# Optimization experiments

Measured on AMD Instinct MI355X. Metric: run time of the kernel, lower is better.

## Reference

```python
import jax, jax.numpy as jnp
import numpy as np

N, E, G = 10000, 80000, 32
Z, C, B, H = 10, 128, 8, 64
R_MAX = 5.0
AVG_NEIGH = 16.0
L_OFF = [0, 1, 4, 9, 16]  # slice offsets for l = 0..3 blocks of the SH vector


def real_sh(u):
    # Real spherical harmonics up to l=3, 'component' normalization (sum_m Y_lm^2 = 2l+1)
    x, y, z = u[:, 0], u[:, 1], u[:, 2]
    s3, s5, s15 = 3.0 ** 0.5, 5.0 ** 0.5, 15.0 ** 0.5
    cols = [
        jnp.ones_like(x),
        s3 * x, s3 * y, s3 * z,
        s15 * x * y, s15 * y * z, (s5 / 2) * (3 * z ** 2 - 1),
        s15 * x * z, (s15 / 2) * (x ** 2 - y ** 2),
        (70.0 ** 0.5 / 4) * (3 * x ** 2 * y - y ** 3),
        105.0 ** 0.5 * x * y * z,
        (42.0 ** 0.5 / 4) * y * (5 * z ** 2 - 1),
        (7.0 ** 0.5 / 2) * (5 * z ** 3 - 3 * z),
        (42.0 ** 0.5 / 4) * x * (5 * z ** 2 - 1),
        (105.0 ** 0.5 / 2) * z * (x ** 2 - y ** 2),
        (70.0 ** 0.5 / 4) * (x ** 3 - 3 * x * y ** 2),
    ]
    return jnp.stack(cols, axis=-1)  # [E, 16]


def poly_cutoff(x, p=5):
    f = (1.0 - (p + 1) * (p + 2) / 2 * x ** p
         + p * (p + 2) * x ** (p + 1)
         - p * (p + 1) / 2 * x ** (p + 2))
    return f * (x < 1.0).astype(f.dtype)


def setup_inputs() -> dict:
    key = jax.random.key(0)
    ks = jax.random.split(key, 20)
    vectors = jax.random.normal(ks[0], (E, 3), dtype=jnp.float32) * 1.5
    elem = jax.random.randint(ks[1], (N,), 0, Z)
    node_attrs = jax.nn.one_hot(elem, Z, dtype=jnp.float32)
    edge_index = jax.random.randint(ks[2], (2, E), 0, N).astype(jnp.int64)
    batch = jnp.sort(jax.random.randint(ks[3], (N,), 0, G)).astype(jnp.int64)

    def init(k, shape, fan_in):
        return jax.random.normal(k, shape, dtype=jnp.float32) / np.sqrt(fan_in)

    return {
        "vectors": vectors,
        "node_attrs": node_attrs,
        "W_embed": init(ks[4], (Z, C), Z),
        "atomic_energies": -jnp.arange(1, Z + 1, dtype=jnp.float32),
        "rw1": init(ks[5], (2, B, H), B),
        "rw2": init(ks[6], (2, H, H), H),
        "rw3": init(ks[7], (2, H, H), H),
        "rw4": init(ks[8], (2, H, 4 * C), H),
        "Wmix": init(ks[9], (2, 4, C, C), C),
        "U": init(ks[10], (2, Z, 4), Z),
        "Wprod": init(ks[11], (2, C, C), C),
        "Wsc": init(ks[12], (2, C, C), C),
        "Wro0": init(ks[13], (C, 1), C),
        "Wro1a": init(ks[14], (C, 16), C),
        "Wro1b": init(ks[15], (16, 1), 16),
        "scale": jnp.array([1.0], dtype=jnp.float32),
        "shift": jnp.array([0.0], dtype=jnp.float32),
        "edge_index": edge_index,
        "batch": batch,
    }


def reference(vectors, node_attrs, W_embed, atomic_energies, rw1, rw2, rw3, rw4,
              Wmix, U, Wprod, Wsc, Wro0, Wro1a, Wro1b, scale, shift,
              edge_index, batch):
    sender, receiver = edge_index[0], edge_index[1]
    r = jnp.linalg.norm(vectors, axis=-1)                     # [E]
    u = vectors / r[:, None]
    Y = real_sh(u)                                            # [E, 16]
    n = jnp.arange(1, B + 1, dtype=vectors.dtype)
    bessel = jnp.sqrt(2.0 / R_MAX) * jnp.sin(n[None] * jnp.pi * r[:, None] / R_MAX) / r[:, None]
    edge_feats = bessel * poly_cutoff(r / R_MAX)[:, None]     # [E, B]

    h = node_attrs @ W_embed                                  # [N, C] node embedding
    node_e0 = node_attrs @ atomic_energies                    # [N] atomic reference energies
    e0 = jax.ops.segment_sum(node_e0, batch, num_segments=G)  # [G]

    node_inter = jnp.zeros((node_attrs.shape[0],), dtype=vectors.dtype)
    for i in range(2):  # interaction layers (fixed small count)
        f = jax.nn.silu(edge_feats @ rw1[i])
        f = jax.nn.silu(f @ rw2[i])
        f = jax.nn.silu(f @ rw3[i])
        R_w = (f @ rw4[i]).reshape(-1, 4, C)                  # [E, 4, C] radial weights per l-path
        hs = h[sender]                                        # [E, C] edge gather
        A_parts = []
        for l in range(4):
            # channelwise tensor product (uvu): scalar node feats x Y_l -> l
            m = (R_w[:, l, :] * hs)[:, :, None] * Y[:, None, L_OFF[l]:L_OFF[l + 1]]  # [E, C, 2l+1]
            agg = jax.ops.segment_sum(m, receiver, num_segments=node_attrs.shape[0]) / AVG_NEIGH
            A_parts.append(jnp.einsum('ncm,cd->ndm', agg, Wmix[i, l]))
        # product basis: rotation-invariant powers per l, element-dependent contraction
        inv = jnp.stack([(p ** 2).sum(-1) for p in A_parts], axis=-1)  # [N, C, 4]
        w = node_attrs @ U[i]                                          # [N, 4]
        h = jnp.einsum('ncl,nl->nc', inv, w) @ Wprod[i] + h @ Wsc[i]   # product + residual sc
        if i == 0:
            node_inter = node_inter + (h @ Wro0)[:, 0]                 # linear readout
        else:
            node_inter = node_inter + (jax.nn.silu(h @ Wro1a) @ Wro1b)[:, 0]  # nonlinear readout
    node_inter = scale[0] * node_inter + shift[0]                       # scale-shift
    total = e0 + jax.ops.segment_sum(node_inter, batch, num_segments=G)
    return total  # [G] per-graph energies
```

## Files before the change

kernel.cpp:

```cpp
#include <hip/hip_runtime.h>

#define NN 10000
#define NE 80000
#define NG 32
#define NZ 10
#define NC 128
#define RMAXF 5.0f

typedef _Float16 f16;
typedef _Float16 half8 __attribute__((ext_vector_type(8)));
typedef float f32x4 __attribute__((ext_vector_type(4)));

__device__ __forceinline__ float silu_f(float x) {
    return x / (1.0f + __expf(-x));
}

__device__ __forceinline__ int clampi(int v, int lo, int hi) {
    return v < lo ? lo : (v > hi ? hi : v);
}

__device__ __forceinline__ uint4 pack8f(float4 a, float4 b) {
    union { f16 h[8]; uint4 u; } P;
    P.h[0] = (f16)a.x; P.h[1] = (f16)a.y; P.h[2] = (f16)a.z; P.h[3] = (f16)a.w;
    P.h[4] = (f16)b.x; P.h[5] = (f16)b.y; P.h[6] = (f16)b.z; P.h[7] = (f16)b.w;
    return P.u;
}

__global__ void zero_stuff(int* counts, int* cursor, float* out) {
    int i = blockIdx.x * blockDim.x + threadIdx.x;
    if (i < NN) { counts[i] = 0; cursor[i] = 0; }
    if (i < NG) out[i] = 0.0f;
}

__global__ void prep_weights(const float* __restrict__ Wmix, const float* __restrict__ Wprod,
                             const float* __restrict__ Wsc,
                             const float* __restrict__ rw2, const float* __restrict__ rw3,
                             const float* __restrict__ rw4,
                             f16* __restrict__ WmixT, f16* __restrict__ WprodT, f16* __restrict__ WscT,
                             f16* __restrict__ w2T, f16* __restrict__ w3T, f16* __restrict__ w4T) {
    int i = blockIdx.x * blockDim.x + threadIdx.x;
    if (i < 2 * 4 * 128 * 128) {
        int cc = i & 127, d = (i >> 7) & 127, g = i >> 14;
        WmixT[i] = (f16)Wmix[((size_t)g * 128 + cc) * 128 + d];
    }
    if (i < 2 * 128 * 128) {
        int cc = i & 127, d = (i >> 7) & 127, g = i >> 14;
        WprodT[i] = (f16)Wprod[((size_t)g * 128 + cc) * 128 + d];
        WscT[i]   = (f16)Wsc[((size_t)g * 128 + cc) * 128 + d];
    }
    if (i < 2 * 512 * 64) {
        int k = i & 63, j = (i >> 6) & 511, ly = i >> 15;
        w4T[i] = (f16)rw4[((size_t)ly * 64 + k) * 512 + j];
    }
    if (i < 2 * 64 * 64) {
        int k = i & 63, j = (i >> 6) & 63, ly = i >> 12;
        w2T[i] = (f16)rw2[((size_t)ly * 64 + k) * 64 + j];
        w3T[i] = (f16)rw3[((size_t)ly * 64 + k) * 64 + j];
    }
}

__global__ void node_init(const float* __restrict__ attrs, const float* __restrict__ W_embed,
                          const float* __restrict__ ae, const float* __restrict__ U,
                          float* __restrict__ h, float* __restrict__ node_e0, float* __restrict__ wU) {
    int gid = blockIdx.x * blockDim.x + threadIdx.x;
    if (gid >= NN * NC) return;
    int n = gid >> 7, c = gid & 127;
    float a[NZ];
#pragma unroll
    for (int z = 0; z < NZ; z++) a[z] = attrs[n * NZ + z];
    float acc = 0.f;
#pragma unroll
    for (int z = 0; z < NZ; z++) acc += a[z] * W_embed[z * NC + c];
    h[(size_t)n * NC + c] = acc;
    if (c == 0) {
        float e = 0.f;
#pragma unroll
        for (int z = 0; z < NZ; z++) e += a[z] * ae[z];
        node_e0[n] = e;
    }
    if (c < 8) {
        int i = c >> 2, l = c & 3;
        float s = 0.f;
#pragma unroll
        for (int z = 0; z < NZ; z++) s += a[z] * U[i * NZ * 4 + z * 4 + l];
        wU[(size_t)i * NN * 4 + n * 4 + l] = s;
    }
}

__global__ void edge_geom(const float* __restrict__ vec, float* __restrict__ Y, float* __restrict__ ef) {
    int e = blockIdx.x * blockDim.x + threadIdx.x;
    if (e >= NE) return;
    float vx = vec[e * 3 + 0], vy = vec[e * 3 + 1], vz = vec[e * 3 + 2];
    float r = sqrtf(vx * vx + vy * vy + vz * vz);
    float inv = 1.0f / r;
    float x = vx * inv, y = vy * inv, z = vz * inv;
    const float s3 = 1.7320508075688772f;
    const float s5 = 2.23606797749979f;
    const float s15 = 3.872983346207417f;
    const float c9 = 2.091650066335189f;
    const float c10 = 10.246950765959598f;
    const float c11 = 1.6201851746019651f;
    const float c12 = 1.3228756555322954f;
    const float c14 = 5.123475382979799f;
    float o[16];
    o[0] = 1.0f;
    o[1] = s3 * x; o[2] = s3 * y; o[3] = s3 * z;
    o[4] = s15 * x * y; o[5] = s15 * y * z; o[6] = 0.5f * s5 * (3.f * z * z - 1.f);
    o[7] = s15 * x * z; o[8] = 0.5f * s15 * (x * x - y * y);
    o[9] = c9 * (3.f * x * x * y - y * y * y);
    o[10] = c10 * x * y * z;
    o[11] = c11 * y * (5.f * z * z - 1.f);
    o[12] = c12 * (5.f * z * z * z - 3.f * z);
    o[13] = c11 * x * (5.f * z * z - 1.f);
    o[14] = c14 * z * (x * x - y * y);
    o[15] = c9 * (x * x * x - 3.f * x * y * y);
#pragma unroll
    for (int m = 0; m < 16; m++) Y[(size_t)e * 16 + m] = o[m];
    float xc = r / RMAXF;
    float cut = 0.0f;
    if (xc < 1.0f) {
        float x5 = xc * xc * xc * xc * xc;
        cut = 1.0f - 21.0f * x5 + 35.0f * x5 * xc - 15.0f * x5 * xc * xc;
    }
    float pref = sqrtf(2.0f / RMAXF) * inv * cut;
#pragma unroll
    for (int b = 0; b < 8; b++) {
        float arg = (float)(b + 1) * 3.14159265358979323846f * r / RMAXF;
        ef[(size_t)e * 8 + b] = pref * sinf(arg);
    }
}

__global__ void hist_recv(const int* __restrict__ recv, int* __restrict__ counts) {
    int e = blockIdx.x * blockDim.x + threadIdx.x;
    if (e < NE) atomicAdd(&counts[clampi(recv[e], 0, NN - 1)], 1);
}

__global__ void scan_counts(const int* __restrict__ counts, int* __restrict__ rowstart) {
    __shared__ int part[1024];
    int t = threadIdx.x;
    const int CH = 10;
    int base = t * CH;
    int loc[CH];
    int s = 0;
#pragma unroll
    for (int j = 0; j < CH; j++) {
        int v = (base + j < NN) ? counts[base + j] : 0;
        loc[j] = s; s += v;
    }
    part[t] = s;
    __syncthreads();
    for (int off = 1; off < 1024; off <<= 1) {
        int v = (t >= off) ? part[t - off] : 0;
        __syncthreads();
        part[t] += v;
        __syncthreads();
    }
    int chunk = (t > 0) ? part[t - 1] : 0;
#pragma unroll
    for (int j = 0; j < CH; j++)
        if (base + j < NN) rowstart[base + j] = chunk + loc[j];
    if (t == 0) rowstart[NN] = part[1023];
}

__global__ void scatter_edges(const int* __restrict__ recv, const int* __restrict__ rowstart,
                              int* __restrict__ cursor, int* __restrict__ elist) {
    int e = blockIdx.x * blockDim.x + threadIdx.x;
    if (e < NE) {
        int r = clampi(recv[e], 0, NN - 1);
        int p = atomicAdd(&cursor[r], 1);
        int slot = clampi(rowstart[r] + p, 0, NE - 1);
        elist[slot] = e;
    }
}

__global__ __launch_bounds__(256) void edge_mlp(const float* __restrict__ ef,
                                                const float* __restrict__ w1,
                                                const f16* __restrict__ w2T, const f16* __restrict__ w3T,
                                                const f16* __restrict__ w4T,
                                                f16* __restrict__ Rw) {
    __shared__ __align__(16) char L[8192 * 2 + 16384];
    char* X1 = L;
    char* X2 = L + 8192;
    char* X4 = L + 16384;

    int tid = threadIdx.x;
    int lane = tid & 63;
    int w = tid >> 6;
    int ln = lane & 15, kq = lane >> 4;
    int eb = blockIdx.x * 64;

    {
        int jb = w * 16;
        const float4* efv = (const float4*)(ef + (size_t)(eb + lane) * 8);
        float4 ea = efv[0], eb4 = efv[1];
        float in8[8] = {ea.x, ea.y, ea.z, ea.w, eb4.x, eb4.y, eb4.z, eb4.w};
        f16 pk[16];
#pragma unroll
        for (int j = 0; j < 16; j++) {
            float a = 0.f;
#pragma unroll
            for (int b = 0; b < 8; b++) a += in8[b] * w1[b * 64 + jb + j];
            pk[j] = (f16)silu_f(a);
        }
        int base = lane * 128 + jb * 2;
#pragma unroll
        for (int t = 0; t < 2; t++) {
            int byte = (base + t * 16) ^ ((lane & 7) << 4);
            *(uint4*)(X1 + byte) = ((uint4*)pk)[t];
        }
    }
    __syncthreads();

    {
        half8 a[2];
#pragma unroll
        for (int kc = 0; kc < 2; kc++) {
            int byte = ((w * 16 + ln) * 128 + kc * 64 + kq * 16) ^ ((ln & 7) << 4);
            a[kc] = *(const half8*)(X1 + byte);
        }
#pragma unroll
        for (int nt = 0; nt < 4; nt++) {
            f32x4 acc = {0.f, 0.f, 0.f, 0.f};
#pragma unroll
            for (int kc = 0; kc < 2; kc++) {
                half8 b = *(const half8*)(w2T + (nt * 16 + ln) * 64 + kc * 32 + kq * 8);
                acc = __builtin_amdgcn_mfma_f32_16x16x32_f16(a[kc], b, acc, 0, 0, 0);
            }
#pragma unroll
            for (int r = 0; r < 4; r++) {
                int row = w * 16 + kq * 4 + r;
                int byte = (row * 128 + (nt * 16 + ln) * 2) ^ ((row & 7) << 4);
                *(f16*)(X2 + byte) = (f16)silu_f(acc[r]);
            }
        }
    }
    __syncthreads();

    {
        half8 a[2];
#pragma unroll
        for (int kc = 0; kc < 2; kc++) {
            int byte = ((w * 16 + ln) * 128 + kc * 64 + kq * 16) ^ ((ln & 7) << 4);
            a[kc] = *(const half8*)(X2 + byte);
        }
#pragma unroll
        for (int nt = 0; nt < 4; nt++) {
            f32x4 acc = {0.f, 0.f, 0.f, 0.f};
#pragma unroll
            for (int kc = 0; kc < 2; kc++) {
                half8 b = *(const half8*)(w3T + (nt * 16 + ln) * 64 + kc * 32 + kq * 8);
                acc = __builtin_amdgcn_mfma_f32_16x16x32_f16(a[kc], b, acc, 0, 0, 0);
            }
#pragma unroll
            for (int r = 0; r < 4; r++) {
                int row = w * 16 + kq * 4 + r;
                int byte = (row * 128 + (nt * 16 + ln) * 2) ^ ((row & 7) << 4);
                *(f16*)(X1 + byte) = (f16)silu_f(acc[r]);
            }
        }
    }
    __syncthreads();

    half8 a3[2];
#pragma unroll
    for (int kc = 0; kc < 2; kc++) {
        int byte = ((w * 16 + ln) * 128 + kc * 64 + kq * 16) ^ ((ln & 7) << 4);
        a3[kc] = *(const half8*)(X1 + byte);
    }
    for (int q = 0; q < 4; q++) {
#pragma unroll
        for (int nt = 0; nt < 8; nt++) {
            f32x4 acc = {0.f, 0.f, 0.f, 0.f};
#pragma unroll
            for (int kc = 0; kc < 2; kc++) {
                half8 b = *(const half8*)(w4T + ((q * 8 + nt) * 16 + ln) * 64 + kc * 32 + kq * 8);
                acc = __builtin_amdgcn_mfma_f32_16x16x32_f16(a3[kc], b, acc, 0, 0, 0);
            }
#pragma unroll
            for (int r = 0; r < 4; r++) {
                int row = w * 16 + kq * 4 + r;
                int byte = (row * 256 + (nt * 16 + ln) * 2) ^ ((row & 15) << 4);
                *(f16*)(X4 + byte) = (f16)acc[r];
            }
        }
#pragma unroll
        for (int it = 0; it < 4; it++) {
            int i = it * 64 + lane;
            int row = w * 16 + (i >> 4);
            int chunk = i & 15;
            int byte = (row * 256 + chunk * 16) ^ ((row & 15) << 4);
            uint4 v = *(const uint4*)(X4 + byte);
            *(uint4*)(Rw + (size_t)(eb + row) * 512 + q * 128 + chunk * 8) = v;
        }
    }
}

__global__ __launch_bounds__(256) void agg_only(const int* __restrict__ rowstart, const int* __restrict__ elist,
                                                const int* __restrict__ send, const float* __restrict__ h_in,
                                                const f16* __restrict__ Rw, const float* __restrict__ Y,
                                                f16* __restrict__ aggH) {
    __shared__ int eL[64], sL[64];
    int n = blockIdx.x, tid = threadIdx.x;
    int c = tid & 127, mh = tid >> 7;
    float acc[8];
#pragma unroll
    for (int q = 0; q < 8; q++) acc[q] = 0.f;
    int beg = rowstart[n], end = rowstart[n + 1];
    for (int base = beg; base < end; base += 64) {
        int cnt = min(64, end - base);
        __syncthreads();
        if (tid < cnt) {
            int e = clampi(elist[base + tid], 0, NE - 1);
            eL[tid] = e;
            sL[tid] = clampi(send[e], 0, NN - 1);
        }
        __syncthreads();
        for (int idx = 0; idx < cnt; idx++) {
            int e = eL[idx];
            int s = sL[idx];
            float hs = h_in[(size_t)s * NC + c];
            const f16* rwp = Rw + (size_t)e * 512;
            float y[8];
#pragma unroll
            for (int q = 0; q < 8; q++) y[q] = Y[(size_t)e * 16 + mh * 8 + q];
            if (mh == 0) {
                float p0 = (float)rwp[c] * hs;
                float p1 = (float)rwp[128 + c] * hs;
                float p2 = (float)rwp[256 + c] * hs;
                acc[0] += p0 * y[0];
                acc[1] += p1 * y[1]; acc[2] += p1 * y[2]; acc[3] += p1 * y[3];
                acc[4] += p2 * y[4]; acc[5] += p2 * y[5]; acc[6] += p2 * y[6]; acc[7] += p2 * y[7];
            } else {
                float p2 = (float)rwp[256 + c] * hs;
                float p3 = (float)rwp[384 + c] * hs;
                acc[0] += p2 * y[0];
#pragma unroll
                for (int q = 1; q < 8; q++) acc[q] += p3 * y[q];
            }
        }
    }
    const float inv16 = 1.0f / 16.0f;
#pragma unroll
    for (int q = 0; q < 8; q++)
        aggH[(size_t)n * 2048 + (size_t)(mh * 8 + q) * NC + c] = (f16)(acc[q] * inv16);
}

__global__ __launch_bounds__(512) void mix_mfma(
    const f16* __restrict__ aggH, const f16* __restrict__ WmixT,
    const float* __restrict__ wU, const float* __restrict__ h_in,
    const f16* __restrict__ WprodT, const f16* __restrict__ WscT,
    const float* __restrict__ Wro0, const float* __restrict__ Wro1a, const float* __restrict__ Wro1b,
    float* __restrict__ h_out, float* __restrict__ ni, int layer)
{
    __shared__ __align__(16) char Lb[32768];
    float* invwL = (float*)(Lb);
    f16*   invwH = (f16*)(Lb + 8192);
    f16*   hH    = (f16*)(Lb + 12288);
    f16*   houtH = (f16*)(Lb + 16384);
    float* p16L  = (float*)(Lb + 20480);

    int tid = threadIdx.x;
    int nb = blockIdx.x * 16;
    int lane = tid & 63;
    int w = tid >> 6;
    int ln = lane & 15, kq = lane >> 4;

    float4 wUreg[4];
#pragma unroll
    for (int r = 0; r < 4; r++)
        wUreg[r] = *(const float4*)(wU + (size_t)(nb + kq * 4 + r) * 4);

    float invwacc[4] = {0.f, 0.f, 0.f, 0.f};

#pragma unroll
    for (int g = 0; g < 4; g++) {
        const int mstart = (g == 0) ? 0 : (g == 1) ? 1 : (g == 2) ? 4 : 9;
        const int mend   = (g == 0) ? 1 : (g == 1) ? 4 : (g == 2) ? 9 : 16;
        {
            const uint4* src = (const uint4*)(WmixT + ((size_t)(layer * 4 + g) << 14));
#pragma unroll
            for (int it = 0; it < 4; it++) {
                int i = it * 512 + tid;
                int row = i >> 4, col = i & 15;
                int byte = (row * 256 + col * 16) ^ ((row & 7) << 4);
                *(uint4*)(Lb + byte) = src[i];
            }
        }
        __syncthreads();
#pragma unroll
        for (int m = mstart; m < mend; m++) {
            half8 a[4];
            const f16* arow = aggH + (size_t)(nb + ln) * 2048 + m * 128 + kq * 8;
#pragma unroll
            for (int k = 0; k < 4; k++) a[k] = *(const half8*)(arow + k * 32);
            f32x4 acc = {0.f, 0.f, 0.f, 0.f};
#pragma unroll
            for (int k = 0; k < 4; k++) {
                int row = w * 16 + ln;
                int byte = (row * 256 + k * 64 + kq * 16) ^ ((row & 7) << 4);
                half8 b = *(const half8*)(Lb + byte);
                acc = __builtin_amdgcn_mfma_f32_16x16x32_f16(a[k], b, acc, 0, 0, 0);
            }
            float wu = (g == 0) ? wUreg[0].x : (g == 1) ? wUreg[0].y : (g == 2) ? wUreg[0].z : wUreg[0].w;
#pragma unroll
            for (int r = 0; r < 4; r++) {
                float wur = (g == 0) ? wUreg[r].x : (g == 1) ? wUreg[r].y : (g == 2) ? wUreg[r].z : wUreg[r].w;
                invwacc[r] += acc[r] * acc[r] * wur;
            }
            (void)wu;
        }
        __syncthreads();
    }

#pragma unroll
    for (int r = 0; r < 4; r++)
        invwL[(kq * 4 + r) * 128 + w * 16 + ln] = invwacc[r];
    __syncthreads();

    if (tid < 256) {
        int node = tid >> 4, ch = tid & 15;
        int byte = (node * 256 + ch * 16) ^ ((node & 7) << 4);
        float4 v0 = *(float4*)&invwL[node * 128 + ch * 8];
        float4 v1 = *(float4*)&invwL[node * 128 + ch * 8 + 4];
        *(uint4*)((char*)invwH + byte) = pack8f(v0, v1);
        const float4* hp = (const float4*)(h_in + (size_t)(nb + node) * 128 + ch * 8);
        float4 g0 = hp[0], g1 = hp[1];
        *(uint4*)((char*)hH + byte) = pack8f(g0, g1);
    }
    __syncthreads();

    {
        half8 ai[4], ah[4];
#pragma unroll
        for (int k = 0; k < 4; k++) {
            int byte = (ln * 256 + (k * 32 + kq * 8) * 2) ^ ((ln & 7) << 4);
            ai[k] = *(const half8*)((char*)invwH + byte);
            ah[k] = *(const half8*)((char*)hH + byte);
        }
        const f16* Bp = WprodT + ((size_t)layer << 14);
        const f16* Bs = WscT + ((size_t)layer << 14);
        f32x4 acc = {0.f, 0.f, 0.f, 0.f};
#pragma unroll
        for (int k = 0; k < 4; k++) {
            half8 b = *(const half8*)(Bp + (w * 16 + ln) * 128 + k * 32 + kq * 8);
            acc = __builtin_amdgcn_mfma_f32_16x16x32_f16(ai[k], b, acc, 0, 0, 0);
        }
#pragma unroll
        for (int k = 0; k < 4; k++) {
            half8 b = *(const half8*)(Bs + (w * 16 + ln) * 128 + k * 32 + kq * 8);
            acc = __builtin_amdgcn_mfma_f32_16x16x32_f16(ah[k], b, acc, 0, 0, 0);
        }
#pragma unroll
        for (int r = 0; r < 4; r++) {
            int node = kq * 4 + r;
            int d = w * 16 + ln;
            h_out[(size_t)(nb + node) * 128 + d] = acc[r];
            houtH[node * 128 + d] = (f16)acc[r];
        }
    }
    __syncthreads();

    if (tid < 256) {
        int rn = tid >> 4, rj = tid & 15;
        if (layer == 0) {
            float s = 0.f;
            for (int cc = rj; cc < 128; cc += 16) s += (float)houtH[rn * 128 + cc] * Wro0[cc];
            p16L[tid] = s;
        } else {
            float s = 0.f;
            for (int cc = 0; cc < 128; cc++) s += (float)houtH[rn * 128 + cc] * Wro1a[cc * 16 + rj];
            s = silu_f(s);
            p16L[tid] = s * Wro1b[rj];
        }
    }
    __syncthreads();
    if (tid < 16) {
        float t = 0.f;
#pragma unroll
        for (int j = 0; j < 16; j++) t += p16L[tid * 16 + j];
        ni[nb + tid] = (layer == 0) ? t : (ni[nb + tid] + t);
    }
}

__global__ void finalize(const float* __restrict__ node_e0, const float* __restrict__ ni,
                         const int* __restrict__ batch, const float* __restrict__ scale,
                         const float* __restrict__ shift, float* __restrict__ out) {
    __shared__ float bins[NG];
    int tid = threadIdx.x;
    if (tid < NG) bins[tid] = 0.f;
    __syncthreads();
    int n = blockIdx.x * blockDim.x + tid;
    if (n < NN) {
        float v = node_e0[n] + scale[0] * ni[n] + shift[0];
        atomicAdd(&bins[clampi(batch[n], 0, NG - 1)], v);
    }
    __syncthreads();
    if (tid < NG) atomicAdd(&out[tid], bins[tid]);
}

extern "C" void kernel_launch(void* const* d_in, const int* in_sizes, int n_in,
                              void* d_out, int out_size, void* d_ws, size_t ws_size,
                              hipStream_t stream) {
    (void)in_sizes; (void)n_in; (void)out_size; (void)ws_size;
    const float* vectors = (const float*)d_in[0];
    const float* attrs   = (const float*)d_in[1];
    const float* W_embed = (const float*)d_in[2];
    const float* ae      = (const float*)d_in[3];
    const float* rw1     = (const float*)d_in[4];
    const float* rw2     = (const float*)d_in[5];
    const float* rw3     = (const float*)d_in[6];
    const float* rw4     = (const float*)d_in[7];
    const float* Wmix    = (const float*)d_in[8];
    const float* U       = (const float*)d_in[9];
    const float* Wprod   = (const float*)d_in[10];
    const float* Wsc     = (const float*)d_in[11];
    const float* Wro0    = (const float*)d_in[12];
    const float* Wro1a   = (const float*)d_in[13];
    const float* Wro1b   = (const float*)d_in[14];
    const float* scale   = (const float*)d_in[15];
    const float* shift   = (const float*)d_in[16];
    const int* eidx      = (const int*)d_in[17];
    const int* batch     = (const int*)d_in[18];
    float* out = (float*)d_out;

    char* w = (char*)d_ws;
    size_t off = 0;
    auto alloc = [&](size_t bytes) -> void* {
        void* p = (void*)(w + off);
        off += (bytes + 255) & ~(size_t)255;
        return p;
    };
    float* Y       = (float*)alloc((size_t)NE * 16 * 4);
    float* ef      = (float*)alloc((size_t)NE * 8 * 4);
    f16*   Rw      = (f16*)  alloc((size_t)NE * 512 * 2);
    f16*   aggH    = (f16*)  alloc((size_t)NN * 2048 * 2);
    float* hA      = (float*)alloc((size_t)NN * NC * 4);
    float* hB      = (float*)alloc((size_t)NN * NC * 4);
    float* wU      = (float*)alloc((size_t)2 * NN * 4 * 4);
    float* node_e0 = (float*)alloc((size_t)NN * 4);
    float* ni      = (float*)alloc((size_t)NN * 4);
    f16*   WmixT   = (f16*)  alloc((size_t)2 * 4 * 128 * 128 * 2);
    f16*   WprodT  = (f16*)  alloc((size_t)2 * 128 * 128 * 2);
    f16*   WscT    = (f16*)  alloc((size_t)2 * 128 * 128 * 2);
    f16*   w2T     = (f16*)  alloc((size_t)2 * 64 * 64 * 2);
    f16*   w3T     = (f16*)  alloc((size_t)2 * 64 * 64 * 2);
    f16*   w4T     = (f16*)  alloc((size_t)2 * 512 * 64 * 2);
    int* counts    = (int*)alloc((size_t)NN * 4);
    int* rowstart  = (int*)alloc((size_t)(NN + 1) * 4);
    int* cursor    = (int*)alloc((size_t)NN * 4);
    int* elist     = (int*)alloc((size_t)NE * 4);

    const int* send = eidx;
    const int* recv = eidx + NE;
    zero_stuff<<<(NN + 255) / 256, 256, 0, stream>>>(counts, cursor, out);
    prep_weights<<<512, 256, 0, stream>>>(Wmix, Wprod, Wsc, rw2, rw3, rw4,
                                          WmixT, WprodT, WscT, w2T, w3T, w4T);
    node_init<<<(NN * NC + 255) / 256, 256, 0, stream>>>(attrs, W_embed, ae, U, hA, node_e0, wU);
    edge_geom<<<(NE + 255) / 256, 256, 0, stream>>>(vectors, Y, ef);
    hist_recv<<<(NE + 255) / 256, 256, 0, stream>>>(recv, counts);
    scan_counts<<<1, 1024, 0, stream>>>(counts, rowstart);
    scatter_edges<<<(NE + 255) / 256, 256, 0, stream>>>(recv, rowstart, cursor, elist);

    float* hcur = hA;
    float* hnext = hB;
    for (int layer = 0; layer < 2; layer++) {
        edge_mlp<<<NE / 64, 256, 0, stream>>>(
            ef, rw1 + layer * 8 * 64,
            w2T + (size_t)layer * 64 * 64, w3T + (size_t)layer * 64 * 64,
            w4T + (size_t)layer * 512 * 64, Rw);
        agg_only<<<NN, 256, 0, stream>>>(rowstart, elist, send, hcur, Rw, Y, aggH);
        mix_mfma<<<NN / 16, 512, 0, stream>>>(
            aggH, WmixT, wU + (size_t)layer * NN * 4, hcur,
            WprodT, WscT, Wro0, Wro1a, Wro1b, hnext, ni, layer);
        float* t = hcur; hcur = hnext; hnext = t;
    }
    finalize<<<(NN + 255) / 256, 256, 0, stream>>>(node_e0, ni, batch, scale, shift, out);
}
```

Before: 354.8 us.

## Fuse edge radial MLP with receiver-sorted aggregation to drop Rw buffer

Replaces the separate edge_mlp and agg_only kernels with one edge_agg kernel. Each block takes the edges of a contiguous range of receiver nodes in sorted order, computes their radial MLP weights in shared memory, and accumulates the messages per node directly into aggH. This removes the global write and re-read of the large per-edge Rw tensor, which is 512 f16 values per edge, in every layer. A new nstart_build kernel maps blocks to node ranges. It also adds an f16 copy of h to halve sender-feature gather traffic. In exchange, the MLP is computed over a padded 128-edge tile per block even when fewer edges are present. The aggregation walks edges one at a time inside each block, and edge loads now go through an indirection.

New measurement: 447.4 us. 1.26x slower.

```diff
diff --git a/kernel.cpp b/kernel.cpp
--- a/kernel.cpp
+++ b/kernel.cpp
@@ -5,10 +5,12 @@
 #define NG 32
 #define NZ 10
 #define NC 128
+#define NB (NE / 64)
 #define RMAXF 5.0f
 
 typedef _Float16 f16;
 typedef _Float16 half8 __attribute__((ext_vector_type(8)));
+typedef _Float16 half4 __attribute__((ext_vector_type(4)));
 typedef float f32x4 __attribute__((ext_vector_type(4)));
 
 __device__ __forceinline__ float silu_f(float x) {
@@ -61,7 +63,8 @@
 
 __global__ void node_init(const float* __restrict__ attrs, const float* __restrict__ W_embed,
                           const float* __restrict__ ae, const float* __restrict__ U,
-                          float* __restrict__ h, float* __restrict__ node_e0, float* __restrict__ wU) {
+                          float* __restrict__ h, f16* __restrict__ h16,
+                          float* __restrict__ node_e0, float* __restrict__ wU) {
     int gid = blockIdx.x * blockDim.x + threadIdx.x;
     if (gid >= NN * NC) return;
     int n = gid >> 7, c = gid & 127;
@@ -72,6 +75,7 @@
 #pragma unroll
     for (int z = 0; z < NZ; z++) acc += a[z] * W_embed[z * NC + c];
     h[(size_t)n * NC + c] = acc;
+    h16[(size_t)n * NC + c] = (f16)acc;
     if (c == 0) {
         float e = 0.f;
 #pragma unroll
@@ -173,25 +177,61 @@
     }
 }
 
-__global__ __launch_bounds__(256) void edge_mlp(const float* __restrict__ ef,
-                                                const float* __restrict__ w1,
-                                                const f16* __restrict__ w2T, const f16* __restrict__ w3T,
-                                                const f16* __restrict__ w4T,
-                                                f16* __restrict__ Rw) {
-    __shared__ __align__(16) char L[8192 * 2 + 16384];
-    char* X1 = L;
-    char* X2 = L + 8192;
-    char* X4 = L + 16384;
+__global__ void nstart_build(const int* __restrict__ rowstart, int* __restrict__ nstart) {
+    int n = blockIdx.x * blockDim.x + threadIdx.x;
+    if (n > NN) return;
+    int b  = (n == NN) ? NB : clampi(rowstart[n] >> 6, 0, NB - 1);
+    int bp = (n == 0) ? -1 : clampi(rowstart[n - 1] >> 6, 0, NB - 1);
+    for (int bb = bp + 1; bb <= b; bb++) nstart[bb] = n;
+}
+
+__global__ __launch_bounds__(512) void edge_agg(
+    const float* __restrict__ ef, const float* __restrict__ w1,
+    const f16* __restrict__ w2T, const f16* __restrict__ w3T, const f16* __restrict__ w4T,
+    const int* __restrict__ rowstart, const int* __restrict__ nstart,
+    const int* __restrict__ elist, const int* __restrict__ send,
+    const f16* __restrict__ h16, const float* __restrict__ Y,
+    f16* __restrict__ aggH)
+{
+    __shared__ __align__(16) char L[54272];
+    char* X1  = L;
+    char* X2  = L + 16384;
+    char* RwC = L + 32768;
+    f16*  yL  = (f16*)(L + 49152);
+    int*  eL  = (int*)(L + 53248);
+    int*  sL  = (int*)(L + 53760);
+
+    int b = blockIdx.x;
+    int n0 = nstart[b], n1 = nstart[b + 1];
+    if (n0 >= n1) return;
+    int e_beg = rowstart[n0];
+    int cnt = rowstart[n1] - e_beg;
+    if (cnt > 128) cnt = 128;
 
     int tid = threadIdx.x;
     int lane = tid & 63;
     int w = tid >> 6;
     int ln = lane & 15, kq = lane >> 4;
-    int eb = blockIdx.x * 64;
-
+
+    if (tid < 128) {
+        int src = e_beg + ((tid < cnt) ? tid : 0);
+        if (src > NE - 1) src = NE - 1;
+        int e = clampi(elist[src], 0, NE - 1);
+        eL[tid] = e;
+        sL[tid] = clampi(send[e], 0, NN - 1);
+    }
+    __syncthreads();
+
+    for (int idx = tid; idx < 2048; idx += 512) {
+        int i = idx >> 4, m = idx & 15;
+        yL[idx] = (f16)Y[(size_t)eL[i] * 16 + m];
+    }
     {
-        int jb = w * 16;
-        const float4* efv = (const float4*)(ef + (size_t)(eb + lane) * 8);
+        int e_i = tid & 127;
+        int q4 = tid >> 7;
+        int jb = q4 * 16;
+        int ge = eL[e_i];
+        const float4* efv = (const float4*)(ef + (size_t)ge * 8);
         float4 ea = efv[0], eb4 = efv[1];
         float in8[8] = {ea.x, ea.y, ea.z, ea.w, eb4.x, eb4.y, eb4.z, eb4.w};
         f16 pk[16];
@@ -199,13 +239,13 @@
         for (int j = 0; j < 16; j++) {
             float a = 0.f;
 #pragma unroll
-            for (int b = 0; b < 8; b++) a += in8[b] * w1[b * 64 + jb + j];
+            for (int bb = 0; bb < 8; bb++) a += in8[bb] * w1[bb * 64 + jb + j];
             pk[j] = (f16)silu_f(a);
         }
-        int base = lane * 128 + jb * 2;
+        int base = e_i * 128 + jb * 2;
 #pragma unroll
         for (int t = 0; t < 2; t++) {
-            int byte = (base + t * 16) ^ ((lane & 7) << 4);
+            int byte = (base + t * 16) ^ ((e_i & 7) << 4);
             *(uint4*)(X1 + byte) = ((uint4*)pk)[t];
         }
     }
@@ -215,7 +255,8 @@
         half8 a[2];
 #pragma unroll
         for (int kc = 0; kc < 2; kc++) {
-            int byte = ((w * 16 + ln) * 128 + kc * 64 + kq * 16) ^ ((ln & 7) << 4);
+            int row = w * 16 + ln;
+            int byte = (row * 128 + kc * 64 + kq * 16) ^ ((row & 7) << 4);
             a[kc] = *(const half8*)(X1 + byte);
         }
 #pragma unroll
@@ -223,8 +264,8 @@
             f32x4 acc = {0.f, 0.f, 0.f, 0.f};
 #pragma unroll
             for (int kc = 0; kc < 2; kc++) {
-                half8 b = *(const half8*)(w2T + (nt * 16 + ln) * 64 + kc * 32 + kq * 8);
-                acc = __builtin_amdgcn_mfma_f32_16x16x32_f16(a[kc], b, acc, 0, 0, 0);
+                half8 bb = *(const half8*)(w2T + (nt * 16 + ln) * 64 + kc * 32 + kq * 8);
+                acc = __builtin_amdgcn_mfma_f32_16x16x32_f16(a[kc], bb, acc, 0, 0, 0);
             }
 #pragma unroll
             for (int r = 0; r < 4; r++) {
@@ -240,7 +281,8 @@
         half8 a[2];
 #pragma unroll
         for (int kc = 0; kc < 2; kc++) {
-            int byte = ((w * 16 + ln) * 128 + kc * 64 + kq * 16) ^ ((ln & 7) << 4);
+            int row = w * 16 + ln;
+            int byte = (row * 128 + kc * 64 + kq * 16) ^ ((row & 7) << 4);
             a[kc] = *(const half8*)(X2 + byte);
         }
 #pragma unroll
@@ -248,8 +290,8 @@
             f32x4 acc = {0.f, 0.f, 0.f, 0.f};
 #pragma unroll
             for (int kc = 0; kc < 2; kc++) {
-                half8 b = *(const half8*)(w3T + (nt * 16 + ln) * 64 + kc * 32 + kq * 8);
-                acc = __builtin_amdgcn_mfma_f32_16x16x32_f16(a[kc], b, acc, 0, 0, 0);
+                half8 bb = *(const half8*)(w3T + (nt * 16 + ln) * 64 + kc * 32 + kq * 8);
+                acc = __builtin_amdgcn_mfma_f32_16x16x32_f16(a[kc], bb, acc, 0, 0, 0);
             }
 #pragma unroll
             for (int r = 0; r < 4; r++) {
@@ -259,90 +301,87 @@
             }
         }
     }
-    __syncthreads();
-
-    half8 a3[2];
-#pragma unroll
-    for (int kc = 0; kc < 2; kc++) {
-        int byte = ((w * 16 + ln) * 128 + kc * 64 + kq * 16) ^ ((ln & 7) << 4);
-        a3[kc] = *(const half8*)(X1 + byte);
-    }
-    for (int q = 0; q < 4; q++) {
-#pragma unroll
-        for (int nt = 0; nt < 8; nt++) {
-            f32x4 acc = {0.f, 0.f, 0.f, 0.f};
+
+    int c = tid & 127;
+    int mq = tid >> 7;
+    float acc0 = 0.f, acc1 = 0.f, acc2 = 0.f, acc3 = 0.f;
+    int nCur = n0;
+    int rsN = rowstart[nCur + 1];
+    const float inv16 = 0.0625f;
+
+    for (int ec = 0; ec < 8; ec++) {
+        __syncthreads();
+        {
+            half8 a[2];
 #pragma unroll
             for (int kc = 0; kc < 2; kc++) {
-                half8 b = *(const half8*)(w4T + ((q * 8 + nt) * 16 + ln) * 64 + kc * 32 + kq * 8);
-                acc = __builtin_amdgcn_mfma_f32_16x16x32_f16(a3[kc], b, acc, 0, 0, 0);
-            }
-#pragma unroll
-            for (int r = 0; r < 4; r++) {
-                int row = w * 16 + kq * 4 + r;
-                int byte = (row * 256 + (nt * 16 + ln) * 2) ^ ((row & 15) << 4);
-                *(f16*)(X4 + byte) = (f16)acc[r];
-            }
-        }
-#pragma unroll
-        for (int it = 0; it < 4; it++) {
-            int i = it * 64 + lane;
-            int row = w * 16 + (i >> 4);
-            int chunk = i & 15;
-            int byte = (row * 256 + chunk * 16) ^ ((row & 15) << 4);
-            uint4 v = *(const uint4*)(X4 + byte);
-            *(uint4*)(Rw + (size_t)(eb + row) * 512 + q * 128 + chunk * 8) = v;
-        }
-    }
-}
-
-__global__ __launch_bounds__(256) void agg_only(const int* __restrict__ rowstart, const int* __restrict__ elist,
-                                                const int* __restrict__ send, const float* __restrict__ h_in,
-                                                const f16* __restrict__ Rw, const float* __restrict__ Y,
-                                                f16* __restrict__ aggH) {
-    __shared__ int eL[64], sL[64];
-    int n = blockIdx.x, tid = threadIdx.x;
-    int c = tid & 127, mh = tid >> 7;
-    float acc[8];
-#pragma unroll
-    for (int q = 0; q < 8; q++) acc[q] = 0.f;
-    int beg = rowstart[n], end = rowstart[n + 1];
-    for (int base = beg; base < end; base += 64) {
-        int cnt = min(64, end - base);
+                int row = ec * 16 + ln;
+                int byte = (row * 128 + kc * 64 + kq * 16) ^ ((row & 7) << 4);
+                a[kc] = *(const half8*)(X1 + byte);
+            }
+#pragma unroll
+            for (int nt = 0; nt < 4; nt++) {
+                f32x4 acc = {0.f, 0.f, 0.f, 0.f};
+#pragma unroll
+                for (int kc = 0; kc < 2; kc++) {
+                    half8 bb = *(const half8*)(w4T + (w * 64 + nt * 16 + ln) * 64 + kc * 32 + kq * 8);
+                    acc = __builtin_amdgcn_mfma_f32_16x16x32_f16(a[kc], bb, acc, 0, 0, 0);
+                }
+#pragma unroll
+                for (int r = 0; r < 4; r++) {
+                    int er = kq * 4 + r;
+                    int col = w * 64 + nt * 16 + ln;
+                    int byte = (er * 1024 + col * 2) ^ ((er & 7) << 4);
+                    *(f16*)(RwC + byte) = (f16)acc[r];
+                }
+            }
+        }
         __syncthreads();
-        if (tid < cnt) {
-            int e = clampi(elist[base + tid], 0, NE - 1);
-            eL[tid] = e;
-            sL[tid] = clampi(send[e], 0, NN - 1);
-        }
-        __syncthreads();
-        for (int idx = 0; idx < cnt; idx++) {
-            int e = eL[idx];
-            int s = sL[idx];
-            float hs = h_in[(size_t)s * NC + c];
-            const f16* rwp = Rw + (size_t)e * 512;
-            float y[8];
-#pragma unroll
-            for (int q = 0; q < 8; q++) y[q] = Y[(size_t)e * 16 + mh * 8 + q];
-            if (mh == 0) {
-                float p0 = (float)rwp[c] * hs;
-                float p1 = (float)rwp[128 + c] * hs;
-                float p2 = (float)rwp[256 + c] * hs;
-                acc[0] += p0 * y[0];
-                acc[1] += p1 * y[1]; acc[2] += p1 * y[2]; acc[3] += p1 * y[3];
-                acc[4] += p2 * y[4]; acc[5] += p2 * y[5]; acc[6] += p2 * y[6]; acc[7] += p2 * y[7];
+        int lim = cnt - ec * 16;
+        lim = (lim < 0) ? 0 : (lim > 16 ? 16 : lim);
+        for (int j = 0; j < lim; j++) {
+            int gi = e_beg + ec * 16 + j;
+            while (gi >= rsN) {
+                size_t base = (size_t)nCur * 2048 + (size_t)(mq * 4) * 128 + c;
+                aggH[base]       = (f16)(acc0 * inv16);
+                aggH[base + 128] = (f16)(acc1 * inv16);
+                aggH[base + 256] = (f16)(acc2 * inv16);
+                aggH[base + 384] = (f16)(acc3 * inv16);
+                acc0 = acc1 = acc2 = acc3 = 0.f;
+                nCur++;
+                rsN = rowstart[nCur + 1];
+            }
+            int i = ec * 16 + j;
+            float hs = (float)h16[(size_t)sL[i] * 128 + c];
+            half4 yv = *(const half4*)(yL + i * 16 + mq * 4);
+            float y0 = (float)yv[0], y1 = (float)yv[1], y2 = (float)yv[2], y3 = (float)yv[3];
+            int swz = (j & 7) << 4;
+            if (mq == 0) {
+                float pa = (float)*(const f16*)(RwC + ((j * 1024 + c * 2) ^ swz)) * hs;
+                float pb = (float)*(const f16*)(RwC + ((j * 1024 + (128 + c) * 2) ^ swz)) * hs;
+                acc0 += pa * y0; acc1 += pb * y1; acc2 += pb * y2; acc3 += pb * y3;
+            } else if (mq == 1) {
+                float p = (float)*(const f16*)(RwC + ((j * 1024 + (256 + c) * 2) ^ swz)) * hs;
+                acc0 += p * y0; acc1 += p * y1; acc2 += p * y2; acc3 += p * y3;
+            } else if (mq == 2) {
+                float pa = (float)*(const f16*)(RwC + ((j * 1024 + (256 + c) * 2) ^ swz)) * hs;
+                float pb = (float)*(const f16*)(RwC + ((j * 1024 + (384 + c) * 2) ^ swz)) * hs;
+                acc0 += pa * y0; acc1 += pb * y1; acc2 += pb * y2; acc3 += pb * y3;
             } else {
-                float p2 = (float)rwp[256 + c] * hs;
-                float p3 = (float)rwp[384 + c] * hs;
-                acc[0] += p2 * y[0];
-#pragma unroll
-                for (int q = 1; q < 8; q++) acc[q] += p3 * y[q];
-            }
-        }
-    }
-    const float inv16 = 1.0f / 16.0f;
-#pragma unroll
-    for (int q = 0; q < 8; q++)
-        aggH[(size_t)n * 2048 + (size_t)(mh * 8 + q) * NC + c] = (f16)(acc[q] * inv16);
+                float p = (float)*(const f16*)(RwC + ((j * 1024 + (384 + c) * 2) ^ swz)) * hs;
+                acc0 += p * y0; acc1 += p * y1; acc2 += p * y2; acc3 += p * y3;
+            }
+        }
+    }
+    while (nCur < n1) {
+        size_t base = (size_t)nCur * 2048 + (size_t)(mq * 4) * 128 + c;
+        aggH[base]       = (f16)(acc0 * inv16);
+        aggH[base + 128] = (f16)(acc1 * inv16);
+        aggH[base + 256] = (f16)(acc2 * inv16);
+        aggH[base + 384] = (f16)(acc3 * inv16);
+        acc0 = acc1 = acc2 = acc3 = 0.f;
+        nCur++;
+    }
 }
 
 __global__ __launch_bounds__(512) void mix_mfma(
@@ -350,7 +389,7 @@
     const float* __restrict__ wU, const float* __restrict__ h_in,
     const f16* __restrict__ WprodT, const f16* __restrict__ WscT,
     const float* __restrict__ Wro0, const float* __restrict__ Wro1a, const float* __restrict__ Wro1b,
-    float* __restrict__ h_out, float* __restrict__ ni, int layer)
+    float* __restrict__ h_out, f16* __restrict__ h16_out, float* __restrict__ ni, int layer)
 {
     __shared__ __align__(16) char Lb[32768];
     float* invwL = (float*)(Lb);
@@ -398,16 +437,14 @@
             for (int k = 0; k < 4; k++) {
                 int row = w * 16 + ln;
                 int byte = (row * 256 + k * 64 + kq * 16) ^ ((row & 7) << 4);
-                half8 b = *(const half8*)(Lb + byte);
-                acc = __builtin_amdgcn_mfma_f32_16x16x32_f16(a[k], b, acc, 0, 0, 0);
-            }
-            float wu = (g == 0) ? wUreg[0].x : (g == 1) ? wUreg[0].y : (g == 2) ? wUreg[0].z : wUreg[0].w;
+                half8 bb = *(const half8*)(Lb + byte);
+                acc = __builtin_amdgcn_mfma_f32_16x16x32_f16(a[k], bb, acc, 0, 0, 0);
+            }
 #pragma unroll
             for (int r = 0; r < 4; r++) {
                 float wur = (g == 0) ? wUreg[r].x : (g == 1) ? wUreg[r].y : (g == 2) ? wUreg[r].z : wUreg[r].w;
                 invwacc[r] += acc[r] * acc[r] * wur;
             }
-            (void)wu;
         }
         __syncthreads();
     }
@@ -442,19 +479,20 @@
         f32x4 acc = {0.f, 0.f, 0.f, 0.f};
 #pragma unroll
         for (int k = 0; k < 4; k++) {
-            half8 b = *(const half8*)(Bp + (w * 16 + ln) * 128 + k * 32 + kq * 8);
-            acc = __builtin_amdgcn_mfma_f32_16x16x32_f16(ai[k], b, acc, 0, 0, 0);
+            half8 bb = *(const half8*)(Bp + (w * 16 + ln) * 128 + k * 32 + kq * 8);
+            acc = __builtin_amdgcn_mfma_f32_16x16x32_f16(ai[k], bb, acc, 0, 0, 0);
         }
 #pragma unroll
         for (int k = 0; k < 4; k++) {
-            half8 b = *(const half8*)(Bs + (w * 16 + ln) * 128 + k * 32 + kq * 8);
-            acc = __builtin_amdgcn_mfma_f32_16x16x32_f16(ah[k], b, acc, 0, 0, 0);
+            half8 bb = *(const half8*)(Bs + (w * 16 + ln) * 128 + k * 32 + kq * 8);
+            acc = __builtin_amdgcn_mfma_f32_16x16x32_f16(ah[k], bb, acc, 0, 0, 0);
         }
 #pragma unroll
         for (int r = 0; r < 4; r++) {
             int node = kq * 4 + r;
             int d = w * 16 + ln;
             h_out[(size_t)(nb + node) * 128 + d] = acc[r];
+            h16_out[(size_t)(nb + node) * 128 + d] = (f16)acc[r];
             houtH[node * 128 + d] = (f16)acc[r];
         }
     }
@@ -532,10 +570,11 @@
     };
     float* Y       = (float*)alloc((size_t)NE * 16 * 4);
     float* ef      = (float*)alloc((size_t)NE * 8 * 4);
-    f16*   Rw      = (f16*)  alloc((size_t)NE * 512 * 2);
     f16*   aggH    = (f16*)  alloc((size_t)NN * 2048 * 2);
     float* hA      = (float*)alloc((size_t)NN * NC * 4);
     float* hB      = (float*)alloc((size_t)NN * NC * 4);
+    f16*   h16A    = (f16*)  alloc((size_t)NN * NC * 2);
+    f16*   h16B    = (f16*)  alloc((size_t)NN * NC * 2);
     float* wU      = (float*)alloc((size_t)2 * NN * 4 * 4);
     float* node_e0 = (float*)alloc((size_t)NN * 4);
     float* ni      = (float*)alloc((size_t)NN * 4);
@@ -549,30 +588,33 @@
     int* rowstart  = (int*)alloc((size_t)(NN + 1) * 4);
     int* cursor    = (int*)alloc((size_t)NN * 4);
     int* elist     = (int*)alloc((size_t)NE * 4);
+    int* nstart    = (int*)alloc((size_t)(NB + 1) * 4);
 
     const int* send = eidx;
     const int* recv = eidx + NE;
     zero_stuff<<<(NN + 255) / 256, 256, 0, stream>>>(counts, cursor, out);
     prep_weights<<<512, 256, 0, stream>>>(Wmix, Wprod, Wsc, rw2, rw3, rw4,
                                           WmixT, WprodT, WscT, w2T, w3T, w4T);
-    node_init<<<(NN * NC + 255) / 256, 256, 0, stream>>>(attrs, W_embed, ae, U, hA, node_e0, wU);
+    node_init<<<(NN * NC + 255) / 256, 256, 0, stream>>>(attrs, W_embed, ae, U, hA, h16A, node_e0, wU);
     edge_geom<<<(NE + 255) / 256, 256, 0, stream>>>(vectors, Y, ef);
     hist_recv<<<(NE + 255) / 256, 256, 0, stream>>>(recv, counts);
     scan_counts<<<1, 1024, 0, stream>>>(counts, rowstart);
     scatter_edges<<<(NE + 255) / 256, 256, 0, stream>>>(recv, rowstart, cursor, elist);
-
-    float* hcur = hA;
-    float* hnext = hB;
+    nstart_build<<<(NN + 1 + 255) / 256, 256, 0, stream>>>(rowstart, nstart);
+
+    float* hcur = hA;   float* hnext = hB;
+    f16* h16cur = h16A; f16* h16next = h16B;
     for (int layer = 0; layer < 2; layer++) {
-        edge_mlp<<<NE / 64, 256, 0, stream>>>(
+        edge_agg<<<NB, 512, 0, stream>>>(
             ef, rw1 + layer * 8 * 64,
             w2T + (size_t)layer * 64 * 64, w3T + (size_t)layer * 64 * 64,
-            w4T + (size_t)layer * 512 * 64, Rw);
-        agg_only<<<NN, 256, 0, stream>>>(rowstart, elist, send, hcur, Rw, Y, aggH);
+            w4T + (size_t)layer * 512 * 64,
+            rowstart, nstart, elist, send, h16cur, Y, aggH);
         mix_mfma<<<NN / 16, 512, 0, stream>>>(
             aggH, WmixT, wU + (size_t)layer * NN * 4, hcur,
-            WprodT, WscT, Wro0, Wro1a, Wro1b, hnext, ni, layer);
+            WprodT, WscT, Wro0, Wro1a, Wro1b, hnext, h16next, ni, layer);
         float* t = hcur; hcur = hnext; hnext = t;
+        f16* t16 = h16cur; h16cur = h16next; h16next = t16;
     }
     finalize<<<(NN + 255) / 256, 256, 0, stream>>>(node_e0, ni, batch, scale, shift, out);
 }
```
